# Kernel tuning notes

Hardware: AMD Instinct MI355X
Metric: run time of the kernel (lower is better)

The kernel has to match this reference:

```python
import jax, jax.numpy as jnp
import numpy as np


def setup_inputs() -> dict:
    key = jax.random.key(0)
    k1, k2, k3, k4 = jax.random.split(key, 4)
    P, BPP, S, DIN, DOUT, LEVELS = 8, 8, 4096, 256, 256, 7  # parscale_n, batch/path, seq, dims, bit levels (2..8)
    x = jax.random.normal(k1, (P * BPP, S, DIN), dtype=jnp.float32)
    # one dequantized weight per bit level (stand-in for mp_weight.get_weight(bits))
    weight_bank = jax.random.normal(k2, (LEVELS, DOUT, DIN), dtype=jnp.float32) * 0.02
    bias = jax.random.normal(k3, (DOUT,), dtype=jnp.float32) * 0.02
    assigned_bits = jax.random.randint(k4, (P,), 0, LEVELS, dtype=jnp.int64)  # index into weight_bank
    return {"x": x, "weight_bank": weight_bank, "bias": bias, "assigned_bits": assigned_bits}


def reference(x, weight_bank, bias, assigned_bits):
    P = assigned_bits.shape[0]
    B, S, Din = x.shape
    bpp = B // P
    xs = x.reshape(P, bpp, S, Din)                 # [P, bpp, S, Din]
    W = weight_bank[assigned_bits]                 # per-path weight select [P, Dout, Din]
    out = jnp.einsum('pbsi,poi->pbso', xs, W) + bias  # grouped dequant-matmul
    return out.reshape(P * bpp, S, -1)
```

## Files before the change

kernel.cpp:

```cpp
#include <hip/hip_runtime.h>


typedef float  floatx4  __attribute__((ext_vector_type(4)));
typedef short  shortx8  __attribute__((ext_vector_type(8)));
typedef unsigned short ushortx4 __attribute__((ext_vector_type(4)));

constexpr int DIN  = 256;
constexpr int DOUT = 256;
constexpr int ROWS_PER_PATH = 8 * 4096;
constexpr int BM   = 64;
constexpr int WBANK_ELEMS = 7 * DOUT * DIN;

__device__ __forceinline__ unsigned short f2bf(float f) {
  union { float f; unsigned u; } c; c.f = f;
  unsigned r = c.u + 0x7fffu + ((c.u >> 16) & 1u);
  return (unsigned short)(r >> 16);
}

__device__ __forceinline__ shortx8 cvt8(floatx4 v0, floatx4 v1) {
  shortx8 h;
  h[0] = (short)f2bf(v0.x); h[1] = (short)f2bf(v0.y);
  h[2] = (short)f2bf(v0.z); h[3] = (short)f2bf(v0.w);
  h[4] = (short)f2bf(v1.x); h[5] = (short)f2bf(v1.y);
  h[6] = (short)f2bf(v1.z); h[7] = (short)f2bf(v1.w);
  return h;
}

__global__ void convert_w_kernel(const float* __restrict__ w,
                                 unsigned short* __restrict__ o, int n4) {
  int i = blockIdx.x * 256 + threadIdx.x;
  if (i < n4) {
    floatx4 v = ((const floatx4*)w)[i];
    ushortx4 h;
    h.x = f2bf(v.x); h.y = f2bf(v.y); h.z = f2bf(v.z); h.w = f2bf(v.w);
    ((ushortx4*)o)[i] = h;
  }
}

template <bool WBF>
__global__ __launch_bounds__(256, 4)
void mp_linear_kernel(const float* __restrict__ x,
                      const void*  __restrict__ wsel,
                      const float* __restrict__ bias,
                      const int*   __restrict__ bits,
                      float* __restrict__ out) {
  const int tid  = threadIdx.x;
  const int row0 = blockIdx.x * BM;
  const int path = row0 / ROWS_PER_PATH;
  const int widx = bits[path];

  const int lane = tid & 63;
  const int wave = tid >> 6;
  const int n0   = wave * 64;
  const int quad = lane >> 4;
  const int l16  = lane & 15;

  const float* __restrict__ xp = x + (size_t)(row0 + l16) * DIN + quad * 8;
  const unsigned short* __restrict__ wbf =
      (const unsigned short*)wsel + (size_t)widx * (DOUT * DIN)
      + (size_t)(n0 + l16) * DIN + quad * 8;
  const float* __restrict__ wf32 =
      (const float*)wsel + (size_t)widx * (DOUT * DIN)
      + (size_t)(n0 + l16) * DIN + quad * 8;

  floatx4 acc[4][4];
#pragma unroll
  for (int i = 0; i < 4; ++i)
#pragma unroll
    for (int j = 0; j < 4; ++j)
      acc[i][j] = (floatx4)0.f;

#pragma unroll 2
  for (int k0 = 0; k0 < DIN; k0 += 32) {
    shortx8 a[4], b[4];
#pragma unroll
    for (int mf = 0; mf < 4; ++mf) {
      const float* p = xp + (size_t)(mf * 16) * DIN + k0;
      a[mf] = cvt8(*(const floatx4*)p, *(const floatx4*)(p + 4));
    }
#pragma unroll
    for (int nf = 0; nf < 4; ++nf) {
      if (WBF) {
        b[nf] = *(const shortx8*)(wbf + (size_t)(nf * 16) * DIN + k0);
      } else {
        const float* p = wf32 + (size_t)(nf * 16) * DIN + k0;
        b[nf] = cvt8(*(const floatx4*)p, *(const floatx4*)(p + 4));
      }
    }
#pragma unroll
    for (int mf = 0; mf < 4; ++mf)
#pragma unroll
      for (int nf = 0; nf < 4; ++nf)
        acc[mf][nf] = __builtin_amdgcn_mfma_f32_16x16x32_bf16(a[mf], b[nf], acc[mf][nf], 0, 0, 0);
  }

  float bv[4];
#pragma unroll
  for (int nf = 0; nf < 4; ++nf)
    bv[nf] = bias[n0 + nf * 16 + l16];

#pragma unroll
  for (int mf = 0; mf < 4; ++mf) {
    const int rbase = row0 + mf * 16 + quad * 4;
#pragma unroll
    for (int nf = 0; nf < 4; ++nf) {
      const int col = n0 + nf * 16 + l16;
      float* o = out + (size_t)rbase * DOUT + col;
#pragma unroll
      for (int r = 0; r < 4; ++r)
        o[(size_t)r * DOUT] = acc[mf][nf][r] + bv[nf];
    }
  }
}

extern "C" void kernel_launch(void* const* d_in, const int* in_sizes, int n_in,
                              void* d_out, int out_size, void* d_ws, size_t ws_size,
                              hipStream_t stream) {
  const float* x     = (const float*)d_in[0];
  const float* wbank = (const float*)d_in[1];
  const float* bias  = (const float*)d_in[2];
  const int*   bits  = (const int*)d_in[3];
  float*       out   = (float*)d_out;

  const int total_rows = in_sizes[0] / DIN;
  const int grid = total_rows / BM;

  const size_t wbf_bytes = (size_t)WBANK_ELEMS * sizeof(unsigned short);
  if (ws_size >= wbf_bytes) {
    unsigned short* wbf = (unsigned short*)d_ws;
    const int n4 = WBANK_ELEMS / 4;
    convert_w_kernel<<<(n4 + 255) / 256, 256, 0, stream>>>(wbank, wbf, n4);
    mp_linear_kernel<true><<<grid, 256, 0, stream>>>(x, wbf, bias, bits, out);
  } else {
    mp_linear_kernel<false><<<grid, 256, 0, stream>>>(x, wbank, bias, bits, out);
  }
}
```

Measured before the change: 557.0 us.

## Stage X tile in swizzled LDS as bf16 and swap MFMA operands for vectorized stores

Each block now loads its 64x256 fp32 X tile with fully coalesced 16-byte loads, converts it once to bf16, and stores it in XOR-swizzled shared memory. Before, each wave re-read X from global memory with strided loads and converted it again. The MFMA operands are swapped (weights as A, X as B), so each lane's accumulator holds four consecutive output columns. This lets the bias add and the output write use float4 vector stores instead of scalar strided ones. The cost is 32KB of LDS per block and a __syncthreads, which may limit occupancy.

Measured after the change: 473.3 us. 1.18x faster.

```diff
diff --git a/kernel.cpp b/kernel.cpp
--- a/kernel.cpp
+++ b/kernel.cpp
@@ -44,6 +44,8 @@
                       const float* __restrict__ bias,
                       const int*   __restrict__ bits,
                       float* __restrict__ out) {
+  __shared__ short xs[BM * DIN];
+
   const int tid  = threadIdx.x;
   const int row0 = blockIdx.x * BM;
   const int path = row0 / ROWS_PER_PATH;
@@ -55,7 +57,27 @@
   const int quad = lane >> 4;
   const int l16  = lane & 15;
 
-  const float* __restrict__ xp = x + (size_t)(row0 + l16) * DIN + quad * 8;
+  {
+    const float* xt = x + (size_t)row0 * DIN;
+    floatx4 v[16];
+#pragma unroll
+    for (int c = 0; c < 8; ++c) {
+      const float* p = xt + (size_t)(tid + c * 256) * 8;
+      v[2 * c]     = *(const floatx4*)p;
+      v[2 * c + 1] = *(const floatx4*)(p + 4);
+    }
+#pragma unroll
+    for (int c = 0; c < 8; ++c) {
+      const int g   = tid + c * 256;
+      const int row = g >> 5;
+      const int col = (g & 31) * 8;
+      int byte = (row * DIN + col) * 2;
+      byte ^= (row & 7) << 4;
+      *(shortx8*)((char*)xs + byte) = cvt8(v[2 * c], v[2 * c + 1]);
+    }
+  }
+  __syncthreads();
+
   const unsigned short* __restrict__ wbf =
       (const unsigned short*)wsel + (size_t)widx * (DOUT * DIN)
       + (size_t)(n0 + l16) * DIN + quad * 8;
@@ -72,43 +94,43 @@
 
 #pragma unroll 2
   for (int k0 = 0; k0 < DIN; k0 += 32) {
-    shortx8 a[4], b[4];
-#pragma unroll
-    for (int mf = 0; mf < 4; ++mf) {
-      const float* p = xp + (size_t)(mf * 16) * DIN + k0;
-      a[mf] = cvt8(*(const floatx4*)p, *(const floatx4*)(p + 4));
-    }
+    shortx8 a[4], xf[4];
 #pragma unroll
     for (int nf = 0; nf < 4; ++nf) {
       if (WBF) {
-        b[nf] = *(const shortx8*)(wbf + (size_t)(nf * 16) * DIN + k0);
+        a[nf] = *(const shortx8*)(wbf + (size_t)(nf * 16) * DIN + k0);
       } else {
         const float* p = wf32 + (size_t)(nf * 16) * DIN + k0;
-        b[nf] = cvt8(*(const floatx4*)p, *(const floatx4*)(p + 4));
+        a[nf] = cvt8(*(const floatx4*)p, *(const floatx4*)(p + 4));
       }
+    }
+#pragma unroll
+    for (int mf = 0; mf < 4; ++mf) {
+      const int row = mf * 16 + l16;
+      int byte = (row * DIN + k0 + quad * 8) * 2;
+      byte ^= (row & 7) << 4;
+      xf[mf] = *(const shortx8*)((const char*)xs + byte);
     }
 #pragma unroll
     for (int mf = 0; mf < 4; ++mf)
 #pragma unroll
       for (int nf = 0; nf < 4; ++nf)
-        acc[mf][nf] = __builtin_amdgcn_mfma_f32_16x16x32_bf16(a[mf], b[nf], acc[mf][nf], 0, 0, 0);
+        acc[mf][nf] = __builtin_amdgcn_mfma_f32_16x16x32_bf16(
+            a[nf], xf[mf], acc[mf][nf], 0, 0, 0);
   }
 
-  float bv[4];
+  floatx4 bv[4];
 #pragma unroll
   for (int nf = 0; nf < 4; ++nf)
-    bv[nf] = bias[n0 + nf * 16 + l16];
+    bv[nf] = *(const floatx4*)(bias + n0 + nf * 16 + quad * 4);
 
 #pragma unroll
   for (int mf = 0; mf < 4; ++mf) {
-    const int rbase = row0 + mf * 16 + quad * 4;
+    float* orow = out + (size_t)(row0 + mf * 16 + l16) * DOUT + n0 + quad * 4;
 #pragma unroll
     for (int nf = 0; nf < 4; ++nf) {
-      const int col = n0 + nf * 16 + l16;
-      float* o = out + (size_t)rbase * DOUT + col;
-#pragma unroll
-      for (int r = 0; r < 4; ++r)
-        o[(size_t)r * DOUT] = acc[mf][nf][r] + bv[nf];
+      floatx4 o4 = acc[mf][nf] + bv[nf];
+      *(floatx4*)(orow + nf * 16) = o4;
     }
   }
 }
```
